# Kernel tuning notes

Measured on AMD Instinct MI355X. Metric: run time of the kernel, lower is better.

The kernel has to match this reference:

```python
import jax, jax.numpy as jnp
import numpy as np
from jax import lax

B, S, D_IN, D_OUT = 2, 1024, 2048, 2048
H, DK, DV, K = 8, 64, 128, 4
CONV_DIM = H * (3 * DK + DV)  # q,k,f each DK per head; v is DV per head
G = H * DV


def _rsa_scan(q, k, v, f, W):
    # q,k,f: [B,S,H,DK]; v: [B,S,H,DV]; W: [H,DV,DV]
    # matrix-valued per-head state St: [B,H,DK,DV], GRU-style gated update
    qs = jnp.moveaxis(q, 1, 0)
    ks = jnp.moveaxis(k, 1, 0)
    vs = jnp.moveaxis(v, 1, 0)
    fs = jnp.moveaxis(f, 1, 0)
    S0 = jnp.zeros((q.shape[0], H, DK, DV), q.dtype)

    def step(St, xs):
        qt, kt, vt, ft = xs
        g = jax.nn.sigmoid(ft)  # [B,H,DK] forget gate
        cand = jnp.tanh(vt[:, :, None, :] + jnp.einsum('bhkv,hvw->bhkw', St, W))
        St = g[..., None] * St + kt[..., None] * cand  # [B,H,DK,DV]
        yt = jnp.einsum('bhk,bhkv->bhv', qt, St)  # readout [B,H,DV]
        return St, yt

    _, ys = lax.scan(step, S0, (qs, ks, vs, fs))
    return jnp.moveaxis(ys, 0, 1)  # [B,S,H,DV]


def setup_inputs() -> dict:
    key = jax.random.key(0)
    ks = jax.random.split(key, 11)
    std = 0.02
    return {
        'x': jax.random.normal(ks[0], (B, S, D_IN), jnp.float32),
        'w_in': jax.random.normal(ks[1], (CONV_DIM + G, D_IN), jnp.float32) * std,
        'b_in': jax.random.normal(ks[2], (CONV_DIM + G,), jnp.float32) * std,
        'conv_w': jax.random.normal(ks[3], (CONV_DIM, 1, K), jnp.float32) * std,
        'conv_b': jax.random.normal(ks[4], (CONV_DIM,), jnp.float32) * std,
        'D': 1.0 + 0.1 * jax.random.normal(ks[5], (H, DV), jnp.float32),
        'state_weight': jax.random.normal(ks[6], (H, DV, DV), jnp.float32) * std,
        'forget_multiplier': 0.1 * jax.random.normal(ks[7], (H,), jnp.float32),
        'forget_bias': 0.1 * jax.random.normal(ks[8], (H, DK), jnp.float32),
        'g_w': 1.0 + 0.1 * jax.random.normal(ks[9], (G,), jnp.float32),
        'w_out': jax.random.normal(ks[10], (D_OUT, G), jnp.float32) * std,
    }


def reference(x, w_in, b_in, conv_w, conv_b, D, state_weight, forget_multiplier, forget_bias, g_w, w_out):
    h = x @ w_in.T + b_in  # input projection [B,S,CONV_DIM+G]
    conv_in, gate = h[..., :CONV_DIM], h[..., CONV_DIM:]
    # causal depthwise conv1d (left pad K-1) + SiLU activation
    xc = jnp.swapaxes(conv_in, 1, 2)  # [B,C,S]
    yc = lax.conv_general_dilated(xc, conv_w, (1,), [(K - 1, 0)], feature_group_count=CONV_DIM)
    yc = jax.nn.silu(yc + conv_b[None, :, None])
    yc = jnp.swapaxes(yc, 1, 2)  # [B,S,CONV_DIM]
    o = 0
    q = yc[..., o:o + H * DK].reshape(B, S, H, DK); o += H * DK
    k = yc[..., o:o + H * DK].reshape(B, S, H, DK); o += H * DK
    v = yc[..., o:o + H * DV].reshape(B, S, H, DV); o += H * DV
    f = yc[..., o:o + H * DK].reshape(B, S, H, DK)
    # p=2 key normalization over head dim (elementwise_affine=False)
    k = k * lax.rsqrt(jnp.sum(k * k, -1, keepdims=True) + 1e-12)
    f = 2.0 * jax.nn.sigmoid(forget_multiplier)[None, None, :, None] * (f + forget_bias[None, None])
    y = _rsa_scan(q, k, v, f, state_weight)  # [B,S,H,DV]
    y = (y + v * D[None, None]).reshape(B, S, G)
    y = y * jax.nn.silu(gate)
    y = y * lax.rsqrt(jnp.mean(y * y, -1, keepdims=True) + 1e-6) * g_w  # RMSNorm
    return y @ w_out.T
```

## Files before the change

### kernel.cpp

```cpp
#include <hip/hip_runtime.h>

typedef unsigned short u16;
typedef unsigned int u32;
typedef __attribute__((ext_vector_type(8))) short short8;
typedef __attribute__((ext_vector_type(4))) float f32x4;

#define N_B 2
#define N_S 1024
#define N_DIN 2048
#define N_DOUT 2048
#define N_H 8
#define N_DK 64
#define N_DV 128
#define N_CONVD 2560
#define N_G 1024
#define N_NH 3584

__device__ __forceinline__ u16 f2bf(float f) {
  u32 u = __float_as_uint(f);
  u32 r = (u + 0x7FFFu + ((u >> 16) & 1u)) >> 16;
  return (u16)r;
}
__device__ __forceinline__ float fsigmoid(float x) {
  return __builtin_amdgcn_rcpf(1.f + __builtin_amdgcn_exp2f(-1.44269504f * x));
}
__device__ __forceinline__ u32 pack_bf16_rhu(float a, float b) {
  u32 ua = __float_as_uint(a) + 0x8000u;
  u32 ub = __float_as_uint(b) + 0x8000u;
  return __builtin_amdgcn_perm(ub, ua, 0x07060302u);
}

__global__ void cvt_kernel(const float* __restrict__ src, u16* __restrict__ dst, int n) {
  int i4 = (blockIdx.x * 256 + threadIdx.x) * 4;
  if (i4 + 3 < n) {
    float4 v = *(const float4*)&src[i4];
    dst[i4 + 0] = f2bf(v.x);
    dst[i4 + 1] = f2bf(v.y);
    dst[i4 + 2] = f2bf(v.z);
    dst[i4 + 3] = f2bf(v.w);
  }
}

__global__ void wtprep_kernel(const float* __restrict__ sw, u16* __restrict__ wtb) {
  int idx = blockIdx.x * 256 + threadIdx.x;
  if (idx >= N_H * 128 * 128) return;
  int h = idx >> 14;
  int rem = idx & 16383;
  int j = rem >> 7, v = rem & 127;
  wtb[idx] = f2bf(sw[((size_t)h * 128 + v) * 128 + j]);
}

__global__ __launch_bounds__(256, 2) void gemm_bt(const u16* __restrict__ A,
                                                  const u16* __restrict__ B,
                                                  const float* __restrict__ bias,
                                                  float* __restrict__ C, int M, int N, int K) {
  const int tid = threadIdx.x;
  const int lane = tid & 63, w = tid >> 6;
  const int u = lane >> 4, m16 = lane & 15;
  const int wm = w & 1, wn = w >> 1;
  const int m0 = blockIdx.y * 128, n0 = blockIdx.x * 128;

  __shared__ __align__(16) u16 As[128 * 32];
  __shared__ __align__(16) u16 Bs[128 * 32];

  f32x4 acc[4][4];
#pragma unroll
  for (int i = 0; i < 4; ++i)
#pragma unroll
    for (int j = 0; j < 4; ++j)
#pragma unroll
      for (int r = 0; r < 4; ++r) acc[i][j][r] = 0.f;

  for (int kk = 0; kk < K; kk += 32) {
#pragma unroll
    for (int q = 0; q < 2; ++q) {
      int chunk = tid + 256 * q;
      int row = chunk >> 2, col = (chunk & 3) * 8;
      *(uint4*)&As[row * 32 + col] = *(const uint4*)&A[(size_t)(m0 + row) * K + kk + col];
      *(uint4*)&Bs[row * 32 + col] = *(const uint4*)&B[(size_t)(n0 + row) * K + kk + col];
    }
    __syncthreads();
    short8 af[4], bfr[4];
#pragma unroll
    for (int i = 0; i < 4; ++i) af[i] = *(const short8*)&As[(64 * wm + 16 * i + m16) * 32 + 8 * u];
#pragma unroll
    for (int i = 0; i < 4; ++i) bfr[i] = *(const short8*)&Bs[(64 * wn + 16 * i + m16) * 32 + 8 * u];
#pragma unroll
    for (int am = 0; am < 4; ++am)
#pragma unroll
      for (int bn = 0; bn < 4; ++bn)
        acc[am][bn] = __builtin_amdgcn_mfma_f32_16x16x32_bf16(af[am], bfr[bn], acc[am][bn], 0, 0, 0);
    __syncthreads();
  }
#pragma unroll
  for (int am = 0; am < 4; ++am)
#pragma unroll
    for (int bn = 0; bn < 4; ++bn) {
      int n = n0 + 64 * wn + 16 * bn + m16;
      float bv = bias ? bias[n] : 0.f;
#pragma unroll
      for (int r = 0; r < 4; ++r) {
        int m = m0 + 64 * wm + 16 * am + 4 * u + r;
        C[(size_t)m * N + n] = acc[am][bn][r] + bv;
      }
    }
}

__global__ void conv_kernel(const float* __restrict__ h, const float* __restrict__ cw,
                            const float* __restrict__ cb, float* __restrict__ SCIN) {
  int gid = blockIdx.x * 256 + threadIdx.x;
  if (gid >= N_B * N_S * N_CONVD) return;
  int c = gid % N_CONVD;
  int bt = gid / N_CONVD;
  int t = bt & 1023, b = bt >> 10;
  float4 wv = *(const float4*)&cw[c * 4];
  const float* wvp = (const float*)&wv;
  float acc = cb[c];
#pragma unroll
  for (int j = 0; j < 4; ++j) {
    int tt = t - 3 + j;
    if (tt >= 0) acc += wvp[j] * h[((size_t)(b * 1024 + tt)) * N_NH + c];
  }
  float yv = acc * fsigmoid(acc);
  int hh, off;
  if (c < 512) { hh = c >> 6; off = c & 63; }
  else if (c < 1024) { int cc = c - 512; hh = cc >> 6; off = 64 + (cc & 63); }
  else if (c < 2048) { int cc = c - 1024; hh = cc >> 7; off = 192 + (cc & 127); }
  else { int cc = c - 2048; hh = cc >> 6; off = 128 + (cc & 63); }
  SCIN[(((size_t)(b * 8 + hh)) * 1024 + t) * 320 + off] = yv;
}

__global__ void prep2_kernel(float* __restrict__ SCIN, const float* __restrict__ fm,
                             const float* __restrict__ fb) {
  int widx = blockIdx.x * 4 + (threadIdx.x >> 6);
  int lane = threadIdx.x & 63;
  int chain = widx >> 10, t = widx & 1023;
  int hh = chain & 7;
  float* base = SCIN + ((size_t)chain * 1024 + t) * 320;
  float kv = base[64 + lane];
  float s = kv * kv;
#pragma unroll
  for (int m = 1; m < 64; m <<= 1) s += __shfl_xor(s, m, 64);
  float inv = __builtin_amdgcn_rsqf(s + 1e-12f);
  base[64 + lane] = kv * inv;
  float fv = base[128 + lane];
  float scale2 = 2.f * fsigmoid(fm[hh]);
  base[128 + lane] = fsigmoid(scale2 * (fv + fb[hh * 64 + lane]));
}

__global__ __launch_bounds__(512, 2) void scan_kernel(const u16* __restrict__ Wtb,
                                                      const float* __restrict__ SCIN,
                                                      float* __restrict__ Ybp) {
  const int tid = threadIdx.x;
  const int lane = tid & 63, wv = tid >> 6;
  const int u = lane >> 4, m16 = lane & 15;
  const int chain = blockIdx.x >> 2;
  const int ig = blockIdx.x & 3;
  const int hh = chain & 7;

  __shared__ __align__(16) u16 Slds[2][16 * 136];

  short8 Wfrag[4];
  {
    const u16* wb = Wtb + ((size_t)hh * 128 + (16 * wv + m16)) * 128 + 8 * u;
#pragma unroll
    for (int kc = 0; kc < 4; ++kc) Wfrag[kc] = *(const short8*)(wb + 32 * kc);
  }

  for (int x = tid; x < 2 * 16 * 136; x += 512) ((u16*)Slds)[x] = 0;

  const float* scin_c = SCIN + (size_t)chain * 1024 * 320;
  float* ybase = Ybp + ((size_t)(chain * 4 + ig)) * 1024 * 128;

  float Sreg[4] = {0.f, 0.f, 0.f, 0.f};

  float qv = scin_c[16 * ig + m16];
  float kv = scin_c[64 + 16 * ig + m16];
  float gv = scin_c[128 + 16 * ig + m16];
  float4 v4 = *(const float4*)&scin_c[192 + 16 * wv + 4 * u];

  __syncthreads();

  for (int t = 0; t < 1024; ++t) {
    const int tn = (t + 1) & 1023;
    const float* pn = scin_c + (size_t)tn * 320;
    float qn = pn[16 * ig + m16];
    float kn = pn[64 + 16 * ig + m16];
    float gn = pn[128 + 16 * ig + m16];
    float4 vn = *(const float4*)&pn[192 + 16 * wv + 4 * u];

    const u16* Sr = Slds[t & 1];
    u16* Sw = Slds[(t + 1) & 1];

    short8 Bfrag[4];
#pragma unroll
    for (int kc = 0; kc < 4; ++kc)
      Bfrag[kc] = *(const short8*)&Sr[m16 * 136 + 32 * kc + 8 * u];

    f32x4 acc0 = {0.f, 0.f, 0.f, 0.f}, acc1 = {0.f, 0.f, 0.f, 0.f};
    acc0 = __builtin_amdgcn_mfma_f32_16x16x32_bf16(Wfrag[0], Bfrag[0], acc0, 0, 0, 0);
    acc1 = __builtin_amdgcn_mfma_f32_16x16x32_bf16(Wfrag[1], Bfrag[1], acc1, 0, 0, 0);
    acc0 = __builtin_amdgcn_mfma_f32_16x16x32_bf16(Wfrag[2], Bfrag[2], acc0, 0, 0, 0);
    acc1 = __builtin_amdgcn_mfma_f32_16x16x32_bf16(Wfrag[3], Bfrag[3], acc1, 0, 0, 0);

    const float* vvp = (const float*)&v4;
    float p[4];
#pragma unroll
    for (int r = 0; r < 4; ++r) {
      float arg = (acc0[r] + acc1[r]) + vvp[r];
      float e = __builtin_amdgcn_exp2f(arg * 2.88539008f);
      float cand = 1.f - 2.f * __builtin_amdgcn_rcpf(e + 1.f);
      Sreg[r] = gv * Sreg[r] + kv * cand;
      p[r] = qv * Sreg[r];
    }

    uint2 pck;
    pck.x = pack_bf16_rhu(Sreg[0], Sreg[1]);
    pck.y = pack_bf16_rhu(Sreg[2], Sreg[3]);
    *(uint2*)&Sw[m16 * 136 + 16 * wv + 4 * u] = pck;

#pragma unroll
    for (int r = 0; r < 4; ++r) {
      float pr = p[r];
      pr += __int_as_float(__builtin_amdgcn_update_dpp(0, __float_as_int(pr), 0x111, 0xF, 0xF, true));
      pr += __int_as_float(__builtin_amdgcn_update_dpp(0, __float_as_int(pr), 0x112, 0xF, 0xF, true));
      pr += __int_as_float(__builtin_amdgcn_update_dpp(0, __float_as_int(pr), 0x114, 0xF, 0xF, true));
      pr += __int_as_float(__builtin_amdgcn_update_dpp(0, __float_as_int(pr), 0x118, 0xF, 0xF, true));
      p[r] = pr;
    }
    if (m16 == 15) {
      f32x4 yo;
      yo[0] = p[0]; yo[1] = p[1]; yo[2] = p[2]; yo[3] = p[3];
      *(f32x4*)(ybase + (size_t)t * 128 + 16 * wv + 4 * u) = yo;
    }

    asm volatile("s_waitcnt lgkmcnt(0)\n\ts_barrier" ::: "memory");

    qv = qn; kv = kn; gv = gn; v4 = vn;
  }
}

__global__ __launch_bounds__(256, 2) void post_kernel(const float* __restrict__ Ybp,
                                                      const float* __restrict__ SCIN,
                                                      const float* __restrict__ h,
                                                      const float* __restrict__ Dp,
                                                      const float* __restrict__ gwv,
                                                      u16* __restrict__ Zb) {
  const int bt = blockIdx.x;
  const int b = bt >> 10, t = bt & 1023;
  const int lane = threadIdx.x & 63, wvi = threadIdx.x >> 6;
  float z[4];
  float ss = 0.f;
#pragma unroll
  for (int c = 0; c < 4; ++c) {
    int j = threadIdx.x + 256 * c;
    int head = j >> 7, dv = j & 127;
    int chain = b * 8 + head;
    float y = 0.f;
#pragma unroll
    for (int igx = 0; igx < 4; ++igx)
      y += Ybp[(((size_t)(chain * 4 + igx)) * 1024 + t) * 128 + dv];
    float v = SCIN[((size_t)chain * 1024 + t) * 320 + 192 + dv];
    float gate = h[((size_t)(b * 1024 + t)) * N_NH + 2560 + j];
    float zz = (y + v * Dp[j]) * (gate * fsigmoid(gate));
    z[c] = zz;
    ss += zz * zz;
  }
#pragma unroll
  for (int m = 1; m < 64; m <<= 1) ss += __shfl_xor(ss, m, 64);
  __shared__ float red[4];
  if (lane == 0) red[wvi] = ss;
  __syncthreads();
  float tot = red[0] + red[1] + red[2] + red[3];
  float scale = __builtin_amdgcn_rsqf(tot * (1.f / 1024.f) + 1e-6f);
#pragma unroll
  for (int c = 0; c < 4; ++c) {
    int j = threadIdx.x + 256 * c;
    Zb[(size_t)(b * 1024 + t) * 1024 + j] = f2bf(z[c] * scale * gwv[j]);
  }
}

extern "C" void kernel_launch(void* const* d_in, const int* in_sizes, int n_in,
                              void* d_out, int out_size, void* d_ws, size_t ws_size,
                              hipStream_t stream) {
  const float* x    = (const float*)d_in[0];
  const float* w_in = (const float*)d_in[1];
  const float* b_in = (const float*)d_in[2];
  const float* cw   = (const float*)d_in[3];
  const float* cb   = (const float*)d_in[4];
  const float* Dp   = (const float*)d_in[5];
  const float* sw   = (const float*)d_in[6];
  const float* fm   = (const float*)d_in[7];
  const float* fb   = (const float*)d_in[8];
  const float* gwv  = (const float*)d_in[9];
  const float* wo   = (const float*)d_in[10];
  float* out = (float*)d_out;

  char* p = (char*)d_ws;
  auto alloc = [&](size_t bytes) {
    char* r = p;
    p += (bytes + 255) & ~(size_t)255;
    return r;
  };
  u16* xb    = (u16*)alloc((size_t)2048 * 2048 * 2);
  u16* wib   = (u16*)alloc((size_t)3584 * 2048 * 2);
  u16* wob   = (u16*)alloc((size_t)2048 * 1024 * 2);
  u16* wtb   = (u16*)alloc((size_t)8 * 128 * 128 * 2);
  float* hbf = (float*)alloc((size_t)2048 * 3584 * 4);
  float* scin= (float*)alloc((size_t)16 * 1024 * 320 * 4);
  float* ybp = (float*)alloc((size_t)64 * 1024 * 128 * 4);
  u16* zb    = (u16*)alloc((size_t)2048 * 1024 * 2);

  cvt_kernel<<<4096, 256, 0, stream>>>(x, xb, 2048 * 2048);
  cvt_kernel<<<7168, 256, 0, stream>>>(w_in, wib, 3584 * 2048);
  cvt_kernel<<<2048, 256, 0, stream>>>(wo, wob, 2048 * 1024);
  wtprep_kernel<<<512, 256, 0, stream>>>(sw, wtb);

  gemm_bt<<<dim3(3584 / 128, 2048 / 128), 256, 0, stream>>>(xb, wib, b_in, hbf, 2048, 3584, 2048);

  conv_kernel<<<(N_B * N_S * N_CONVD) / 256, 256, 0, stream>>>(hbf, cw, cb, scin);
  prep2_kernel<<<(16 * 1024) / 4, 256, 0, stream>>>(scin, fm, fb);

  scan_kernel<<<64, 512, 0, stream>>>(wtb, scin, ybp);

  post_kernel<<<2048, 256, 0, stream>>>(ybp, scin, hbf, Dp, gwv, zb);

  gemm_bt<<<dim3(2048 / 128, 2048 / 128), 256, 0, stream>>>(zb, wob, nullptr, out, 2048, 2048, 1024);
}
```

Measured before the change: 651.3 us.

## Halve scan workgroup size, fold tanh scale into weights, defer readout reduction

The recurrent scan now runs 4 waves per block instead of 8, with each wave computing two 16-row output tiles so that fewer waves take part in each per-step barrier. The tanh exp2 scale factor is folded into the bf16 state weight and the v channels (post_kernel divides the D term back out). v is also fed as the MFMA accumulator init, which removes per-step adds. The DPP readout reduction and the global store are deferred by one timestep so they overlap the next step's LDS load. Native v_cvt_pk_bf16_f32 replaces the manual round-half-up pack. The trade-off is more registers per thread and a little extra rounding from scaling the weight before bf16 conversion.

```diff
diff --git a/kernel.cpp b/kernel.cpp
--- a/kernel.cpp
+++ b/kernel.cpp
@@ -16,6 +16,9 @@
 #define N_G 1024
 #define N_NH 3584
 
+#define C_E2 2.88539008f
+#define C_E2_INV 0.34657359f
+
 __device__ __forceinline__ u16 f2bf(float f) {
   u32 u = __float_as_uint(f);
   u32 r = (u + 0x7FFFu + ((u >> 16) & 1u)) >> 16;
@@ -24,10 +27,17 @@
 __device__ __forceinline__ float fsigmoid(float x) {
   return __builtin_amdgcn_rcpf(1.f + __builtin_amdgcn_exp2f(-1.44269504f * x));
 }
-__device__ __forceinline__ u32 pack_bf16_rhu(float a, float b) {
-  u32 ua = __float_as_uint(a) + 0x8000u;
-  u32 ub = __float_as_uint(b) + 0x8000u;
-  return __builtin_amdgcn_perm(ub, ua, 0x07060302u);
+__device__ __forceinline__ u32 cvt_pk_bf16(float lo, float hi) {
+  u32 r;
+  asm("v_cvt_pk_bf16_f32 %0, %1, %2" : "=v"(r) : "v"(lo), "v"(hi));
+  return r;
+}
+__device__ __forceinline__ float row16_prefix_sum(float pr) {
+  pr += __int_as_float(__builtin_amdgcn_update_dpp(0, __float_as_int(pr), 0x111, 0xF, 0xF, true));
+  pr += __int_as_float(__builtin_amdgcn_update_dpp(0, __float_as_int(pr), 0x112, 0xF, 0xF, true));
+  pr += __int_as_float(__builtin_amdgcn_update_dpp(0, __float_as_int(pr), 0x114, 0xF, 0xF, true));
+  pr += __int_as_float(__builtin_amdgcn_update_dpp(0, __float_as_int(pr), 0x118, 0xF, 0xF, true));
+  return pr;
 }
 
 __global__ void cvt_kernel(const float* __restrict__ src, u16* __restrict__ dst, int n) {
@@ -47,7 +57,7 @@
   int h = idx >> 14;
   int rem = idx & 16383;
   int j = rem >> 7, v = rem & 127;
-  wtb[idx] = f2bf(sw[((size_t)h * 128 + v) * 128 + j]);
+  wtb[idx] = f2bf(C_E2 * sw[((size_t)h * 128 + v) * 128 + j]);
 }
 
 __global__ __launch_bounds__(256, 2) void gemm_bt(const u16* __restrict__ A,
@@ -122,6 +132,7 @@
     if (tt >= 0) acc += wvp[j] * h[((size_t)(b * 1024 + tt)) * N_NH + c];
   }
   float yv = acc * fsigmoid(acc);
+  if (c >= 1024 && c < 2048) yv *= C_E2;
   int hh, off;
   if (c < 512) { hh = c >> 6; off = c & 63; }
   else if (c < 1024) { int cc = c - 512; hh = cc >> 6; off = 64 + (cc & 63); }
@@ -148,7 +159,7 @@
   base[128 + lane] = fsigmoid(scale2 * (fv + fb[hh * 64 + lane]));
 }
 
-__global__ __launch_bounds__(512, 2) void scan_kernel(const u16* __restrict__ Wtb,
+__global__ __launch_bounds__(256, 1) void scan_kernel(const u16* __restrict__ Wtb,
                                                       const float* __restrict__ SCIN,
                                                       float* __restrict__ Ybp) {
   const int tid = threadIdx.x;
@@ -160,83 +171,107 @@
 
   __shared__ __align__(16) u16 Slds[2][16 * 136];
 
-  short8 Wfrag[4];
-  {
-    const u16* wb = Wtb + ((size_t)hh * 128 + (16 * wv + m16)) * 128 + 8 * u;
-#pragma unroll
-    for (int kc = 0; kc < 4; ++kc) Wfrag[kc] = *(const short8*)(wb + 32 * kc);
-  }
-
-  for (int x = tid; x < 2 * 16 * 136; x += 512) ((u16*)Slds)[x] = 0;
+  short8 Wf[2][4];
+#pragma unroll
+  for (int T = 0; T < 2; ++T) {
+    const u16* wb = Wtb + ((size_t)hh * 128 + (32 * wv + 16 * T + m16)) * 128 + 8 * u;
+#pragma unroll
+    for (int kc = 0; kc < 4; ++kc) Wf[T][kc] = *(const short8*)(wb + 32 * kc);
+  }
+
+  for (int x = tid; x < 2 * 16 * 136; x += 256) ((u16*)Slds)[x] = 0;
 
   const float* scin_c = SCIN + (size_t)chain * 1024 * 320;
   float* ybase = Ybp + ((size_t)(chain * 4 + ig)) * 1024 * 128;
 
-  float Sreg[4] = {0.f, 0.f, 0.f, 0.f};
+  float Sreg[2][4] = {{0.f, 0.f, 0.f, 0.f}, {0.f, 0.f, 0.f, 0.f}};
+  float pp[2][4];
 
   float qv = scin_c[16 * ig + m16];
   float kv = scin_c[64 + 16 * ig + m16];
   float gv = scin_c[128 + 16 * ig + m16];
-  float4 v4 = *(const float4*)&scin_c[192 + 16 * wv + 4 * u];
+  f32x4 cv0 = *(const f32x4*)&scin_c[192 + 32 * wv + 4 * u];
+  f32x4 cv1 = *(const f32x4*)&scin_c[192 + 32 * wv + 16 + 4 * u];
 
   __syncthreads();
 
   for (int t = 0; t < 1024; ++t) {
+    const u16* Sr = Slds[t & 1];
+    u16* Sw = Slds[(t + 1) & 1];
+
+    short8 Bf[4];
+#pragma unroll
+    for (int kc = 0; kc < 4; ++kc)
+      Bf[kc] = *(const short8*)&Sr[m16 * 136 + 32 * kc + 8 * u];
+
     const int tn = (t + 1) & 1023;
     const float* pn = scin_c + (size_t)tn * 320;
     float qn = pn[16 * ig + m16];
     float kn = pn[64 + 16 * ig + m16];
     float gn = pn[128 + 16 * ig + m16];
-    float4 vn = *(const float4*)&pn[192 + 16 * wv + 4 * u];
-
-    const u16* Sr = Slds[t & 1];
-    u16* Sw = Slds[(t + 1) & 1];
-
-    short8 Bfrag[4];
-#pragma unroll
-    for (int kc = 0; kc < 4; ++kc)
-      Bfrag[kc] = *(const short8*)&Sr[m16 * 136 + 32 * kc + 8 * u];
-
-    f32x4 acc0 = {0.f, 0.f, 0.f, 0.f}, acc1 = {0.f, 0.f, 0.f, 0.f};
-    acc0 = __builtin_amdgcn_mfma_f32_16x16x32_bf16(Wfrag[0], Bfrag[0], acc0, 0, 0, 0);
-    acc1 = __builtin_amdgcn_mfma_f32_16x16x32_bf16(Wfrag[1], Bfrag[1], acc1, 0, 0, 0);
-    acc0 = __builtin_amdgcn_mfma_f32_16x16x32_bf16(Wfrag[2], Bfrag[2], acc0, 0, 0, 0);
-    acc1 = __builtin_amdgcn_mfma_f32_16x16x32_bf16(Wfrag[3], Bfrag[3], acc1, 0, 0, 0);
-
-    const float* vvp = (const float*)&v4;
-    float p[4];
+    f32x4 cn0 = *(const f32x4*)&pn[192 + 32 * wv + 4 * u];
+    f32x4 cn1 = *(const f32x4*)&pn[192 + 32 * wv + 16 + 4 * u];
+
+    if (t) {
+#pragma unroll
+      for (int T = 0; T < 2; ++T)
+#pragma unroll
+        for (int r = 0; r < 4; ++r) pp[T][r] = row16_prefix_sum(pp[T][r]);
+      if (m16 == 15) {
+        f32x4 y0, y1;
+#pragma unroll
+        for (int r = 0; r < 4; ++r) { y0[r] = pp[0][r]; y1[r] = pp[1][r]; }
+        *(f32x4*)(ybase + (size_t)(t - 1) * 128 + 32 * wv + 4 * u) = y0;
+        *(f32x4*)(ybase + (size_t)(t - 1) * 128 + 32 * wv + 16 + 4 * u) = y1;
+      }
+    }
+
+    f32x4 a0 = cv0, b0 = {0.f, 0.f, 0.f, 0.f};
+    f32x4 a1 = cv1, b1 = {0.f, 0.f, 0.f, 0.f};
+    a0 = __builtin_amdgcn_mfma_f32_16x16x32_bf16(Wf[0][0], Bf[0], a0, 0, 0, 0);
+    a1 = __builtin_amdgcn_mfma_f32_16x16x32_bf16(Wf[1][0], Bf[0], a1, 0, 0, 0);
+    b0 = __builtin_amdgcn_mfma_f32_16x16x32_bf16(Wf[0][1], Bf[1], b0, 0, 0, 0);
+    b1 = __builtin_amdgcn_mfma_f32_16x16x32_bf16(Wf[1][1], Bf[1], b1, 0, 0, 0);
+    a0 = __builtin_amdgcn_mfma_f32_16x16x32_bf16(Wf[0][2], Bf[2], a0, 0, 0, 0);
+    a1 = __builtin_amdgcn_mfma_f32_16x16x32_bf16(Wf[1][2], Bf[2], a1, 0, 0, 0);
+    b0 = __builtin_amdgcn_mfma_f32_16x16x32_bf16(Wf[0][3], Bf[3], b0, 0, 0, 0);
+    b1 = __builtin_amdgcn_mfma_f32_16x16x32_bf16(Wf[1][3], Bf[3], b1, 0, 0, 0);
+
 #pragma unroll
     for (int r = 0; r < 4; ++r) {
-      float arg = (acc0[r] + acc1[r]) + vvp[r];
-      float e = __builtin_amdgcn_exp2f(arg * 2.88539008f);
-      float cand = 1.f - 2.f * __builtin_amdgcn_rcpf(e + 1.f);
-      Sreg[r] = gv * Sreg[r] + kv * cand;
-      p[r] = qv * Sreg[r];
+      float e0 = __builtin_amdgcn_exp2f(a0[r] + b0[r]);
+      float c0 = __builtin_fmaf(-2.f, __builtin_amdgcn_rcpf(e0 + 1.f), 1.f);
+      Sreg[0][r] = __builtin_fmaf(gv, Sreg[0][r], kv * c0);
+      pp[0][r] = qv * Sreg[0][r];
+      float e1 = __builtin_amdgcn_exp2f(a1[r] + b1[r]);
+      float c1 = __builtin_fmaf(-2.f, __builtin_amdgcn_rcpf(e1 + 1.f), 1.f);
+      Sreg[1][r] = __builtin_fmaf(gv, Sreg[1][r], kv * c1);
+      pp[1][r] = qv * Sreg[1][r];
     }
 
-    uint2 pck;
-    pck.x = pack_bf16_rhu(Sreg[0], Sreg[1]);
-    pck.y = pack_bf16_rhu(Sreg[2], Sreg[3]);
-    *(uint2*)&Sw[m16 * 136 + 16 * wv + 4 * u] = pck;
-
-#pragma unroll
-    for (int r = 0; r < 4; ++r) {
-      float pr = p[r];
-      pr += __int_as_float(__builtin_amdgcn_update_dpp(0, __float_as_int(pr), 0x111, 0xF, 0xF, true));
-      pr += __int_as_float(__builtin_amdgcn_update_dpp(0, __float_as_int(pr), 0x112, 0xF, 0xF, true));
-      pr += __int_as_float(__builtin_amdgcn_update_dpp(0, __float_as_int(pr), 0x114, 0xF, 0xF, true));
-      pr += __int_as_float(__builtin_amdgcn_update_dpp(0, __float_as_int(pr), 0x118, 0xF, 0xF, true));
-      p[r] = pr;
-    }
-    if (m16 == 15) {
-      f32x4 yo;
-      yo[0] = p[0]; yo[1] = p[1]; yo[2] = p[2]; yo[3] = p[3];
-      *(f32x4*)(ybase + (size_t)t * 128 + 16 * wv + 4 * u) = yo;
-    }
+    uint2 w0, w1;
+    w0.x = cvt_pk_bf16(Sreg[0][0], Sreg[0][1]);
+    w0.y = cvt_pk_bf16(Sreg[0][2], Sreg[0][3]);
+    w1.x = cvt_pk_bf16(Sreg[1][0], Sreg[1][1]);
+    w1.y = cvt_pk_bf16(Sreg[1][2], Sreg[1][3]);
+    *(uint2*)&Sw[m16 * 136 + 32 * wv + 4 * u] = w0;
+    *(uint2*)&Sw[m16 * 136 + 32 * wv + 16 + 4 * u] = w1;
 
     asm volatile("s_waitcnt lgkmcnt(0)\n\ts_barrier" ::: "memory");
 
-    qv = qn; kv = kn; gv = gn; v4 = vn;
+    qv = qn; kv = kn; gv = gn; cv0 = cn0; cv1 = cn1;
+  }
+
+#pragma unroll
+  for (int T = 0; T < 2; ++T)
+#pragma unroll
+    for (int r = 0; r < 4; ++r) pp[T][r] = row16_prefix_sum(pp[T][r]);
+  if (m16 == 15) {
+    f32x4 y0, y1;
+#pragma unroll
+    for (int r = 0; r < 4; ++r) { y0[r] = pp[0][r]; y1[r] = pp[1][r]; }
+    *(f32x4*)(ybase + (size_t)1023 * 128 + 32 * wv + 4 * u) = y0;
+    *(f32x4*)(ybase + (size_t)1023 * 128 + 32 * wv + 16 + 4 * u) = y1;
   }
 }
 
@@ -262,7 +297,7 @@
       y += Ybp[(((size_t)(chain * 4 + igx)) * 1024 + t) * 128 + dv];
     float v = SCIN[((size_t)chain * 1024 + t) * 320 + 192 + dv];
     float gate = h[((size_t)(b * 1024 + t)) * N_NH + 2560 + j];
-    float zz = (y + v * Dp[j]) * (gate * fsigmoid(gate));
+    float zz = (y + v * (Dp[j] * C_E2_INV)) * (gate * fsigmoid(gate));
     z[c] = zz;
     ss += zz * zz;
   }
@@ -321,7 +356,7 @@
   conv_kernel<<<(N_B * N_S * N_CONVD) / 256, 256, 0, stream>>>(hbf, cw, cb, scin);
   prep2_kernel<<<(16 * 1024) / 4, 256, 0, stream>>>(scin, fm, fb);
 
-  scan_kernel<<<64, 512, 0, stream>>>(wtb, scin, ybp);
+  scan_kernel<<<64, 256, 0, stream>>>(wtb, scin, ybp);
 
   post_kernel<<<2048, 256, 0, stream>>>(ybp, scin, hbf, Dp, gwv, zb);
 
```

Measured after the change: 852.8 us. +30.9%, slower.

## Fold tanh scale into weights, defer readout reduction, pack two scan units per block

Applied to the files above, without the earlier changes.

The 2*log2(e) factor of tanh is folded into the state weight and the v channels so the MFMA accumulator starts at the scaled v and the per-step multiply disappears; post_kernel undoes the scaling on v. The readout reduction and store for step t are deferred into step t+1 to overlap with the MFMA, v_cvt_pk_bf16_f32 replaces the manual bf16 packing, and two independent scan units share a 1024-thread block. Packing two units per block halves the block count but makes them share a barrier, so each unit may stall on the other. Bf16 rounding now applies to the scaled weights and uses round-to-nearest-even.

```diff
diff --git a/kernel.cpp b/kernel.cpp
--- a/kernel.cpp
+++ b/kernel.cpp
@@ -16,6 +16,9 @@
 #define N_G 1024
 #define N_NH 3584
 
+#define C_E2 2.88539008f
+#define C_E2_INV 0.34657359f
+
 __device__ __forceinline__ u16 f2bf(float f) {
   u32 u = __float_as_uint(f);
   u32 r = (u + 0x7FFFu + ((u >> 16) & 1u)) >> 16;
@@ -24,10 +27,17 @@
 __device__ __forceinline__ float fsigmoid(float x) {
   return __builtin_amdgcn_rcpf(1.f + __builtin_amdgcn_exp2f(-1.44269504f * x));
 }
-__device__ __forceinline__ u32 pack_bf16_rhu(float a, float b) {
-  u32 ua = __float_as_uint(a) + 0x8000u;
-  u32 ub = __float_as_uint(b) + 0x8000u;
-  return __builtin_amdgcn_perm(ub, ua, 0x07060302u);
+__device__ __forceinline__ u32 cvt_pk_bf16(float lo, float hi) {
+  u32 r;
+  asm("v_cvt_pk_bf16_f32 %0, %1, %2" : "=v"(r) : "v"(lo), "v"(hi));
+  return r;
+}
+__device__ __forceinline__ float row16_prefix_sum(float pr) {
+  pr += __int_as_float(__builtin_amdgcn_update_dpp(0, __float_as_int(pr), 0x111, 0xF, 0xF, true));
+  pr += __int_as_float(__builtin_amdgcn_update_dpp(0, __float_as_int(pr), 0x112, 0xF, 0xF, true));
+  pr += __int_as_float(__builtin_amdgcn_update_dpp(0, __float_as_int(pr), 0x114, 0xF, 0xF, true));
+  pr += __int_as_float(__builtin_amdgcn_update_dpp(0, __float_as_int(pr), 0x118, 0xF, 0xF, true));
+  return pr;
 }
 
 __global__ void cvt_kernel(const float* __restrict__ src, u16* __restrict__ dst, int n) {
@@ -47,7 +57,7 @@
   int h = idx >> 14;
   int rem = idx & 16383;
   int j = rem >> 7, v = rem & 127;
-  wtb[idx] = f2bf(sw[((size_t)h * 128 + v) * 128 + j]);
+  wtb[idx] = f2bf(C_E2 * sw[((size_t)h * 128 + v) * 128 + j]);
 }
 
 __global__ __launch_bounds__(256, 2) void gemm_bt(const u16* __restrict__ A,
@@ -122,6 +132,7 @@
     if (tt >= 0) acc += wvp[j] * h[((size_t)(b * 1024 + tt)) * N_NH + c];
   }
   float yv = acc * fsigmoid(acc);
+  if (c >= 1024 && c < 2048) yv *= C_E2;
   int hh, off;
   if (c < 512) { hh = c >> 6; off = c & 63; }
   else if (c < 1024) { int cc = c - 512; hh = cc >> 6; off = 64 + (cc & 63); }
@@ -148,17 +159,21 @@
   base[128 + lane] = fsigmoid(scale2 * (fv + fb[hh * 64 + lane]));
 }
 
-__global__ __launch_bounds__(512, 2) void scan_kernel(const u16* __restrict__ Wtb,
-                                                      const float* __restrict__ SCIN,
-                                                      float* __restrict__ Ybp) {
+__global__ __launch_bounds__(1024, 1) void scan_kernel(const u16* __restrict__ Wtb,
+                                                       const float* __restrict__ SCIN,
+                                                       float* __restrict__ Ybp) {
   const int tid = threadIdx.x;
-  const int lane = tid & 63, wv = tid >> 6;
+  const int lane = tid & 63;
+  const int wave = tid >> 6;
+  const int unit = wave >> 3;
+  const int wv = wave & 7;
   const int u = lane >> 4, m16 = lane & 15;
-  const int chain = blockIdx.x >> 2;
-  const int ig = blockIdx.x & 3;
+  const int gu = blockIdx.x * 2 + unit;
+  const int chain = gu >> 2;
+  const int ig = gu & 3;
   const int hh = chain & 7;
 
-  __shared__ __align__(16) u16 Slds[2][16 * 136];
+  __shared__ __align__(16) u16 Slds[2][2][16 * 136];
 
   short8 Wfrag[4];
   {
@@ -167,76 +182,79 @@
     for (int kc = 0; kc < 4; ++kc) Wfrag[kc] = *(const short8*)(wb + 32 * kc);
   }
 
-  for (int x = tid; x < 2 * 16 * 136; x += 512) ((u16*)Slds)[x] = 0;
+  for (int x = tid; x < 2 * 2 * 16 * 136; x += 1024) ((u16*)Slds)[x] = 0;
 
   const float* scin_c = SCIN + (size_t)chain * 1024 * 320;
   float* ybase = Ybp + ((size_t)(chain * 4 + ig)) * 1024 * 128;
 
   float Sreg[4] = {0.f, 0.f, 0.f, 0.f};
+  float pp[4];
 
   float qv = scin_c[16 * ig + m16];
   float kv = scin_c[64 + 16 * ig + m16];
   float gv = scin_c[128 + 16 * ig + m16];
-  float4 v4 = *(const float4*)&scin_c[192 + 16 * wv + 4 * u];
+  f32x4 cv = *(const f32x4*)&scin_c[192 + 16 * wv + 4 * u];
 
   __syncthreads();
 
   for (int t = 0; t < 1024; ++t) {
+    const u16* Sr = Slds[unit][t & 1];
+    u16* Sw = Slds[unit][(t + 1) & 1];
+
+    short8 Bfrag[4];
+#pragma unroll
+    for (int kc = 0; kc < 4; ++kc)
+      Bfrag[kc] = *(const short8*)&Sr[m16 * 136 + 32 * kc + 8 * u];
+
     const int tn = (t + 1) & 1023;
     const float* pn = scin_c + (size_t)tn * 320;
     float qn = pn[16 * ig + m16];
     float kn = pn[64 + 16 * ig + m16];
     float gn = pn[128 + 16 * ig + m16];
-    float4 vn = *(const float4*)&pn[192 + 16 * wv + 4 * u];
-
-    const u16* Sr = Slds[t & 1];
-    u16* Sw = Slds[(t + 1) & 1];
-
-    short8 Bfrag[4];
-#pragma unroll
-    for (int kc = 0; kc < 4; ++kc)
-      Bfrag[kc] = *(const short8*)&Sr[m16 * 136 + 32 * kc + 8 * u];
-
-    f32x4 acc0 = {0.f, 0.f, 0.f, 0.f}, acc1 = {0.f, 0.f, 0.f, 0.f};
-    acc0 = __builtin_amdgcn_mfma_f32_16x16x32_bf16(Wfrag[0], Bfrag[0], acc0, 0, 0, 0);
-    acc1 = __builtin_amdgcn_mfma_f32_16x16x32_bf16(Wfrag[1], Bfrag[1], acc1, 0, 0, 0);
-    acc0 = __builtin_amdgcn_mfma_f32_16x16x32_bf16(Wfrag[2], Bfrag[2], acc0, 0, 0, 0);
-    acc1 = __builtin_amdgcn_mfma_f32_16x16x32_bf16(Wfrag[3], Bfrag[3], acc1, 0, 0, 0);
-
-    const float* vvp = (const float*)&v4;
-    float p[4];
+    f32x4 cn = *(const f32x4*)&pn[192 + 16 * wv + 4 * u];
+
+    if (t) {
+#pragma unroll
+      for (int r = 0; r < 4; ++r) pp[r] = row16_prefix_sum(pp[r]);
+      if (m16 == 15) {
+        f32x4 yo;
+#pragma unroll
+        for (int r = 0; r < 4; ++r) yo[r] = pp[r];
+        *(f32x4*)(ybase + (size_t)(t - 1) * 128 + 16 * wv + 4 * u) = yo;
+      }
+    }
+
+    f32x4 a0 = cv, a1 = {0.f, 0.f, 0.f, 0.f};
+    a0 = __builtin_amdgcn_mfma_f32_16x16x32_bf16(Wfrag[0], Bfrag[0], a0, 0, 0, 0);
+    a1 = __builtin_amdgcn_mfma_f32_16x16x32_bf16(Wfrag[1], Bfrag[1], a1, 0, 0, 0);
+    a0 = __builtin_amdgcn_mfma_f32_16x16x32_bf16(Wfrag[2], Bfrag[2], a0, 0, 0, 0);
+    a1 = __builtin_amdgcn_mfma_f32_16x16x32_bf16(Wfrag[3], Bfrag[3], a1, 0, 0, 0);
+
 #pragma unroll
     for (int r = 0; r < 4; ++r) {
-      float arg = (acc0[r] + acc1[r]) + vvp[r];
-      float e = __builtin_amdgcn_exp2f(arg * 2.88539008f);
-      float cand = 1.f - 2.f * __builtin_amdgcn_rcpf(e + 1.f);
-      Sreg[r] = gv * Sreg[r] + kv * cand;
-      p[r] = qv * Sreg[r];
+      float e = __builtin_amdgcn_exp2f(a0[r] + a1[r]);
+      float c = __builtin_fmaf(-2.f, __builtin_amdgcn_rcpf(e + 1.f), 1.f);
+      Sreg[r] = __builtin_fmaf(gv, Sreg[r], kv * c);
+      pp[r] = qv * Sreg[r];
     }
 
-    uint2 pck;
-    pck.x = pack_bf16_rhu(Sreg[0], Sreg[1]);
-    pck.y = pack_bf16_rhu(Sreg[2], Sreg[3]);
-    *(uint2*)&Sw[m16 * 136 + 16 * wv + 4 * u] = pck;
-
-#pragma unroll
-    for (int r = 0; r < 4; ++r) {
-      float pr = p[r];
-      pr += __int_as_float(__builtin_amdgcn_update_dpp(0, __float_as_int(pr), 0x111, 0xF, 0xF, true));
-      pr += __int_as_float(__builtin_amdgcn_update_dpp(0, __float_as_int(pr), 0x112, 0xF, 0xF, true));
-      pr += __int_as_float(__builtin_amdgcn_update_dpp(0, __float_as_int(pr), 0x114, 0xF, 0xF, true));
-      pr += __int_as_float(__builtin_amdgcn_update_dpp(0, __float_as_int(pr), 0x118, 0xF, 0xF, true));
-      p[r] = pr;
-    }
-    if (m16 == 15) {
-      f32x4 yo;
-      yo[0] = p[0]; yo[1] = p[1]; yo[2] = p[2]; yo[3] = p[3];
-      *(f32x4*)(ybase + (size_t)t * 128 + 16 * wv + 4 * u) = yo;
-    }
+    uint2 w0;
+    w0.x = cvt_pk_bf16(Sreg[0], Sreg[1]);
+    w0.y = cvt_pk_bf16(Sreg[2], Sreg[3]);
+    *(uint2*)&Sw[m16 * 136 + 16 * wv + 4 * u] = w0;
 
     asm volatile("s_waitcnt lgkmcnt(0)\n\ts_barrier" ::: "memory");
 
-    qv = qn; kv = kn; gv = gn; v4 = vn;
+    qv = qn; kv = kn; gv = gn; cv = cn;
+  }
+
+#pragma unroll
+  for (int r = 0; r < 4; ++r) pp[r] = row16_prefix_sum(pp[r]);
+  if (m16 == 15) {
+    f32x4 yo;
+#pragma unroll
+    for (int r = 0; r < 4; ++r) yo[r] = pp[r];
+    *(f32x4*)(ybase + (size_t)1023 * 128 + 16 * wv + 4 * u) = yo;
   }
 }
 
@@ -262,7 +280,7 @@
       y += Ybp[(((size_t)(chain * 4 + igx)) * 1024 + t) * 128 + dv];
     float v = SCIN[((size_t)chain * 1024 + t) * 320 + 192 + dv];
     float gate = h[((size_t)(b * 1024 + t)) * N_NH + 2560 + j];
-    float zz = (y + v * Dp[j]) * (gate * fsigmoid(gate));
+    float zz = (y + v * (Dp[j] * C_E2_INV)) * (gate * fsigmoid(gate));
     z[c] = zz;
     ss += zz * zz;
   }
@@ -321,7 +339,7 @@
   conv_kernel<<<(N_B * N_S * N_CONVD) / 256, 256, 0, stream>>>(hbf, cw, cb, scin);
   prep2_kernel<<<(16 * 1024) / 4, 256, 0, stream>>>(scin, fm, fb);
 
-  scan_kernel<<<64, 512, 0, stream>>>(wtb, scin, ybp);
+  scan_kernel<<<32, 1024, 0, stream>>>(wtb, scin, ybp);
 
   post_kernel<<<2048, 256, 0, stream>>>(ybp, scin, hbf, Dp, gwv, zb);
 
```

Measured after the change: 930.4 us. 42.9% more time.
